# Kernel optimization log

Hardware: AMD Instinct MI355X
Metric: run time of the kernel (lower is better)

## Reference

```python
import jax, jax.numpy as jnp
import numpy as np

D_MODEL = 1024
NUM_HEADS = 16
HEAD_DIM = D_MODEL // NUM_HEADS


def setup_inputs() -> dict:
    key = jax.random.key(0)
    ks = jax.random.split(key, 6)
    B, S = 2, 2048
    w_scale = 1.0 / np.sqrt(D_MODEL)  # keep logits O(1) so the naive exp-softmax is stable
    return {
        "x": jax.random.normal(ks[0], (B, S, D_MODEL), dtype=jnp.float32),
        "y": jax.random.normal(ks[1], (B, S, D_MODEL), dtype=jnp.float32),
        "mask": jnp.zeros((S, S), dtype=jnp.float32),
        "Wq": jax.random.normal(ks[2], (D_MODEL, D_MODEL), dtype=jnp.float32) * w_scale,
        "Wk": jax.random.normal(ks[3], (D_MODEL, D_MODEL), dtype=jnp.float32) * w_scale,
        "Wv": jax.random.normal(ks[4], (D_MODEL, D_MODEL), dtype=jnp.float32) * w_scale,
        "Wo": jax.random.normal(ks[5], (D_MODEL, D_MODEL), dtype=jnp.float32) * w_scale,
    }


def _naive_softmax(s):
    # faithful to nirmalya_softmax: plain exp, sum + eps, no max subtraction
    p1 = jnp.exp(s)
    p2 = jnp.sum(p1, axis=-1, keepdims=True) + 1e-10
    return p1 / p2


def reference(x, y, mask, Wq, Wk, Wv, Wo):
    B, S, _ = x.shape
    # nn.Linear(bias=False): t @ W.T ; split heads -> [B, H, S, Dh]
    def split_heads(t):
        return t.reshape(B, S, NUM_HEADS, HEAD_DIM).transpose(0, 2, 1, 3)

    k = split_heads(x @ Wk.T)
    v = split_heads(x @ Wv.T)
    q = split_heads(y @ Wq.T)

    scores = jnp.einsum("bhqd,bhkd->bhqk", q, k) / np.sqrt(HEAD_DIM)
    scores = scores + mask  # [S,S] broadcasts over [B,H,S,S] (same math as permute-add-permute)
    attn = _naive_softmax(scores)
    out = jnp.einsum("bhqk,bhkd->bhqd", attn, v)  # [B,H,S,Dh]
    out = out.transpose(0, 2, 1, 3).reshape(B, S, D_MODEL)
    return out @ Wo.T
```

## Files before the change

### kernel.cpp

```cpp
#include <hip/hip_runtime.h>
#include <stdint.h>

typedef unsigned short u16;
typedef __attribute__((ext_vector_type(4))) float f32x4;
typedef __attribute__((ext_vector_type(8))) __bf16 bf16x8;
typedef __attribute__((ext_vector_type(4))) u16 u16x4;

#define AS1 __attribute__((address_space(1)))
#define AS3 __attribute__((address_space(3)))
#define GLOAD_LDS16(gp, lp) \
  __builtin_amdgcn_global_load_lds((const AS1 void*)(gp), (AS3 void*)(lp), 16, 0, 0)

__device__ __forceinline__ u16 f2bf(float f) {
  union { float f; unsigned u; } v; v.f = f;
  return (u16)((v.u + 0x7FFFu + ((v.u >> 16) & 1u)) >> 16);
}

__global__ __launch_bounds__(256) void convert_all(
    const float* __restrict__ x, const float* __restrict__ y,
    const float* __restrict__ wq, const float* __restrict__ wk,
    const float* __restrict__ wv, const float* __restrict__ wo,
    u16* __restrict__ xb, u16* __restrict__ yb, u16* __restrict__ wqb,
    u16* __restrict__ wkb, u16* __restrict__ wvb, u16* __restrict__ wob) {
  size_t i = (size_t)blockIdx.x * 256 + threadIdx.x;
  const float* src; u16* dst; float scale = 1.0f; size_t off;
  if (i < (size_t)(1u << 20)) { src = x; dst = xb; off = i; }
  else if (i < (size_t)(2u << 20)) { src = y; dst = yb; off = i - (1u << 20); }
  else {
    size_t j = i - (size_t)(2u << 20);
    unsigned w = (unsigned)(j >> 18); off = j & ((1u << 18) - 1);
    if (w == 0)      { src = wq; dst = wqb; scale = 0.125f; }
    else if (w == 1) { src = wk; dst = wkb; }
    else if (w == 2) { src = wv; dst = wvb; }
    else             { src = wo; dst = wob; }
  }
  f32x4 v = ((const f32x4*)src)[off];
  u16x4 r;
  r.x = f2bf(v.x * scale); r.y = f2bf(v.y * scale);
  r.z = f2bf(v.z * scale); r.w = f2bf(v.w * scale);
  ((u16x4*)dst)[off] = r;
}

template <int MODE>
__global__ __launch_bounds__(256, 2) void gemm_bt(
    const u16* __restrict__ A, const u16* __restrict__ Bt,
    void* __restrict__ C, int M, int N) {
  constexpr int K = 1024;
  __shared__ __align__(16) u16 As[128 * 32];
  __shared__ __align__(16) u16 Bs[128 * 32];
  const int tid = threadIdx.x;
  const int wave = tid >> 6, lane = tid & 63;
  const int l15 = lane & 15, quad = lane >> 4;
  const int tm = blockIdx.y * 128, tn = blockIdx.x * 128;
  const int wr = wave >> 1, wc = wave & 1;

  const int srow = wave * 32 + (lane >> 2);
  const int scol = (lane & 3) * 8;
  const u16* Ag = A + (size_t)(tm + srow) * K + scol;
  const u16* Bg = Bt + (size_t)(tn + srow) * K + scol;
  u16* Asl0 = &As[(wave * 2 + 0) * 512];
  u16* Asl1 = &As[(wave * 2 + 1) * 512];
  u16* Bsl0 = &Bs[(wave * 2 + 0) * 512];
  u16* Bsl1 = &Bs[(wave * 2 + 1) * 512];

  f32x4 acc[4][4] = {};

  for (int k0 = 0; k0 < K; k0 += 32) {
    __syncthreads();
    GLOAD_LDS16(Ag + k0, Asl0);
    GLOAD_LDS16(Ag + 16 * K + k0, Asl1);
    GLOAD_LDS16(Bg + k0, Bsl0);
    GLOAD_LDS16(Bg + 16 * K + k0, Bsl1);
    __syncthreads();
    bf16x8 af[4], bfr[4];
#pragma unroll
    for (int mi = 0; mi < 4; ++mi)
      af[mi] = *(const bf16x8*)&As[(wr * 64 + mi * 16 + l15) * 32 + quad * 8];
#pragma unroll
    for (int ni = 0; ni < 4; ++ni)
      bfr[ni] = *(const bf16x8*)&Bs[(wc * 64 + ni * 16 + l15) * 32 + quad * 8];
#pragma unroll
    for (int mi = 0; mi < 4; ++mi)
#pragma unroll
      for (int ni = 0; ni < 4; ++ni)
        acc[mi][ni] = __builtin_amdgcn_mfma_f32_16x16x32_bf16(
            af[mi], bfr[ni], acc[mi][ni], 0, 0, 0);
  }

#pragma unroll
  for (int mi = 0; mi < 4; ++mi) {
#pragma unroll
    for (int ni = 0; ni < 4; ++ni) {
#pragma unroll
      for (int r = 0; r < 4; ++r) {
        int gm = tm + wr * 64 + mi * 16 + quad * 4 + r;
        int gn = tn + wc * 64 + ni * 16 + l15;
        float val = acc[mi][ni][r];
        if (MODE == 0) {
          int b = gm >> 11, s = gm & 2047, h = gn >> 6, dh = gn & 63;
          ((u16*)C)[(((size_t)(b * 16 + h) * 2048 + s) << 6) + dh] = f2bf(val);
        } else if (MODE == 1) {
          int h = gm >> 6, dh = gm & 63, b = gn >> 11, s = gn & 2047;
          ((u16*)C)[(((size_t)(b * 16 + h) * 64 + dh) << 11) + s] = f2bf(val);
        } else {
          ((float*)C)[(size_t)gm * 1024 + gn] = val;
        }
      }
    }
  }
  (void)M; (void)N;
}

__global__ __launch_bounds__(256, 2) void attn_kernel(
    const u16* __restrict__ Qw, const u16* __restrict__ Kw,
    const u16* __restrict__ Vtw, const float* __restrict__ mask,
    u16* __restrict__ Ow) {
  constexpr int S = 2048;
  __shared__ __align__(16) u16 Ks[128 * 64];
  __shared__ __align__(16) u16 Vs[64 * 128];
  __shared__ __align__(16) u16 Ps[128 * 136];
  const int tid = threadIdx.x;
  const int wave = tid >> 6, lane = tid & 63;
  const int l15 = lane & 15, quad = lane >> 4;
  const int qt = blockIdx.x, h = blockIdx.y, b = blockIdx.z;
  const size_t head = ((size_t)(b * 16 + h)) * S * 64;

  bf16x8 aq[2][2];
#pragma unroll
  for (int mi = 0; mi < 2; ++mi)
#pragma unroll
    for (int kq = 0; kq < 2; ++kq)
      aq[mi][kq] = *(const bf16x8*)&Qw[head +
          (size_t)(qt * 128 + wave * 32 + mi * 16 + l15) * 64 + kq * 32 + quad * 8];

  __bf16 one_bf = (__bf16)1.0f;
  bf16x8 ones = {one_bf, one_bf, one_bf, one_bf, one_bf, one_bf, one_bf, one_bf};

  f32x4 oa[2][4] = {};
  f32x4 den[2] = {};

  const int krow = lane >> 3, kcol = (lane & 7) * 8;
  const int vrow = lane >> 4, vcol = (lane & 15) * 8;

  for (int kt = 0; kt < S; kt += 128) {
    __syncthreads();
#pragma unroll
    for (int c = 0; c < 4; ++c) {
      int g = wave * 4 + c;
      GLOAD_LDS16(&Kw[head + (size_t)(kt + g * 8 + krow) * 64 + kcol], &Ks[g * 512]);
    }
#pragma unroll
    for (int c = 0; c < 4; ++c) {
      int g = wave * 4 + c;
      GLOAD_LDS16(&Vtw[head + (size_t)(g * 4 + vrow) * S + kt + vcol], &Vs[g * 512]);
    }
    __syncthreads();

    f32x4 sa[2][8] = {};
#pragma unroll
    for (int kq = 0; kq < 2; ++kq) {
#pragma unroll
      for (int ni = 0; ni < 8; ++ni) {
        bf16x8 bk = *(const bf16x8*)&Ks[(ni * 16 + l15) * 64 + kq * 32 + quad * 8];
#pragma unroll
        for (int mi = 0; mi < 2; ++mi)
          sa[mi][ni] = __builtin_amdgcn_mfma_f32_16x16x32_bf16(
              aq[mi][kq], bk, sa[mi][ni], 0, 0, 0);
      }
    }

#pragma unroll
    for (int mi = 0; mi < 2; ++mi) {
#pragma unroll
      for (int ni = 0; ni < 8; ++ni) {
        int prow = wave * 32 + mi * 16 + quad * 4;
        int pcol = ni * 16 + l15;
        const float* mp = mask + (size_t)(qt * 128 + prow) * S + kt + pcol;
#pragma unroll
        for (int r = 0; r < 4; ++r) {
          float p = __expf(sa[mi][ni][r] + mp[(size_t)r * S]);
          Ps[(prow + r) * 136 + pcol] = f2bf(p);
        }
      }
    }

#pragma unroll
    for (int kq2 = 0; kq2 < 4; ++kq2) {
      bf16x8 ap[2];
#pragma unroll
      for (int mi = 0; mi < 2; ++mi)
        ap[mi] = *(const bf16x8*)&Ps[(wave * 32 + mi * 16 + l15) * 136 + kq2 * 32 + quad * 8];
#pragma unroll
      for (int ni = 0; ni < 4; ++ni) {
        bf16x8 bv = *(const bf16x8*)&Vs[(ni * 16 + l15) * 128 + kq2 * 32 + quad * 8];
#pragma unroll
        for (int mi = 0; mi < 2; ++mi)
          oa[mi][ni] = __builtin_amdgcn_mfma_f32_16x16x32_bf16(
              ap[mi], bv, oa[mi][ni], 0, 0, 0);
      }
#pragma unroll
      for (int mi = 0; mi < 2; ++mi)
        den[mi] = __builtin_amdgcn_mfma_f32_16x16x32_bf16(
            ap[mi], ones, den[mi], 0, 0, 0);
    }
  }

#pragma unroll
  for (int mi = 0; mi < 2; ++mi) {
#pragma unroll
    for (int ni = 0; ni < 4; ++ni) {
#pragma unroll
      for (int r = 0; r < 4; ++r) {
        int srow = qt * 128 + wave * 32 + mi * 16 + quad * 4 + r;
        int dh = ni * 16 + l15;
        float val = oa[mi][ni][r] / (den[mi][r] + 1e-10f);
        Ow[((size_t)(b * S + srow) << 10) + h * 64 + dh] = f2bf(val);
      }
    }
  }
}

extern "C" void kernel_launch(void* const* d_in, const int* in_sizes, int n_in,
                              void* d_out, int out_size, void* d_ws, size_t ws_size,
                              hipStream_t stream) {
  const float* x    = (const float*)d_in[0];
  const float* y    = (const float*)d_in[1];
  const float* mask = (const float*)d_in[2];
  const float* Wq   = (const float*)d_in[3];
  const float* Wk   = (const float*)d_in[4];
  const float* Wv   = (const float*)d_in[5];
  const float* Wo   = (const float*)d_in[6];
  char* ws = (char*)d_ws;
  const size_t MB = (size_t)1 << 20;
  u16* xb  = (u16*)(ws + 0  * MB);
  u16* yb  = (u16*)(ws + 8  * MB);
  u16* wqb = (u16*)(ws + 16 * MB);
  u16* wkb = (u16*)(ws + 18 * MB);
  u16* wvb = (u16*)(ws + 20 * MB);
  u16* wob = (u16*)(ws + 22 * MB);
  u16* Qw  = (u16*)(ws + 24 * MB);
  u16* Kw  = (u16*)(ws + 32 * MB);
  u16* Vtw = (u16*)(ws + 40 * MB);
  u16* Ow  = (u16*)(ws + 48 * MB);

  convert_all<<<12288, 256, 0, stream>>>(x, y, Wq, Wk, Wv, Wo,
                                         xb, yb, wqb, wkb, wvb, wob);
  gemm_bt<0><<<dim3(8, 32), 256, 0, stream>>>(yb, wqb, (void*)Qw, 4096, 1024);
  gemm_bt<0><<<dim3(8, 32), 256, 0, stream>>>(xb, wkb, (void*)Kw, 4096, 1024);
  gemm_bt<1><<<dim3(32, 8), 256, 0, stream>>>(wvb, xb, (void*)Vtw, 1024, 4096);
  attn_kernel<<<dim3(16, 16, 2), 256, 0, stream>>>(Qw, Kw, Vtw, mask, Ow);
  gemm_bt<2><<<dim3(8, 32), 256, 0, stream>>>(Ow, wob, d_out, 4096, 1024);
  (void)in_sizes; (void)n_in; (void)out_size; (void)ws_size;
}
```

Baseline: 288.8 us.

## Fuse QKV GEMMs, swizzle LDS, shrink attention tiles, vectorize mask and packing

Merges the three Q/K/V projection GEMMs into one launch with a z-dimension selector. Adds XOR swizzles to the GEMM and attention LDS layouts to avoid bank conflicts. Restructures attention to 64 query rows per block (16 per wave), computing S^T so that each lane holds four consecutive keys; this allows vectorized float4 mask loads issued before the barrier and packed bf16 stores into P. It also uses the hardware packed bf16 conversion when available and raises occupancy to 3 blocks per SM, at the cost of less K/V reuse per block and doubling the number of blocks.

```diff
diff --git a/kernel.cpp b/kernel.cpp
--- a/kernel.cpp
+++ b/kernel.cpp
@@ -3,6 +3,7 @@
 
 typedef unsigned short u16;
 typedef __attribute__((ext_vector_type(4))) float f32x4;
+typedef __attribute__((ext_vector_type(2))) __bf16 bf16x2;
 typedef __attribute__((ext_vector_type(8))) __bf16 bf16x8;
 typedef __attribute__((ext_vector_type(4))) u16 u16x4;
 
@@ -14,6 +15,17 @@
 __device__ __forceinline__ u16 f2bf(float f) {
   union { float f; unsigned u; } v; v.f = f;
   return (u16)((v.u + 0x7FFFu + ((v.u >> 16) & 1u)) >> 16);
+}
+
+__device__ __forceinline__ u16x4 pack4(float a, float b, float c, float d) {
+#if __has_builtin(__builtin_amdgcn_cvt_pk_bf16_f32)
+  union { struct { bf16x2 lo, hi; } p; u16x4 v; } u;
+  u.p.lo = __builtin_amdgcn_cvt_pk_bf16_f32(a, b);
+  u.p.hi = __builtin_amdgcn_cvt_pk_bf16_f32(c, d);
+  return u.v;
+#else
+  u16x4 r; r.x = f2bf(a); r.y = f2bf(b); r.z = f2bf(c); r.w = f2bf(d); return r;
+#endif
 }
 
 __global__ __launch_bounds__(256) void convert_all(
@@ -35,35 +47,24 @@
     else             { src = wo; dst = wob; }
   }
   f32x4 v = ((const f32x4*)src)[off];
-  u16x4 r;
-  r.x = f2bf(v.x * scale); r.y = f2bf(v.y * scale);
-  r.z = f2bf(v.z * scale); r.w = f2bf(v.w * scale);
-  ((u16x4*)dst)[off] = r;
-}
-
-template <int MODE>
-__global__ __launch_bounds__(256, 2) void gemm_bt(
-    const u16* __restrict__ A, const u16* __restrict__ Bt,
-    void* __restrict__ C, int M, int N) {
+  ((u16x4*)dst)[off] = pack4(v.x * scale, v.y * scale, v.z * scale, v.w * scale);
+}
+
+__device__ __forceinline__ void gemm_core(
+    const u16* __restrict__ A, const u16* __restrict__ Bt, int tm, int tn,
+    u16* As, u16* Bs, f32x4 acc[4][4], int wave, int lane) {
   constexpr int K = 1024;
-  __shared__ __align__(16) u16 As[128 * 32];
-  __shared__ __align__(16) u16 Bs[128 * 32];
-  const int tid = threadIdx.x;
-  const int wave = tid >> 6, lane = tid & 63;
-  const int l15 = lane & 15, quad = lane >> 4;
-  const int tm = blockIdx.y * 128, tn = blockIdx.x * 128;
+  const int l15 = lane & 15, quad = lane >> 4;
   const int wr = wave >> 1, wc = wave & 1;
-
-  const int srow = wave * 32 + (lane >> 2);
-  const int scol = (lane & 3) * 8;
-  const u16* Ag = A + (size_t)(tm + srow) * K + scol;
-  const u16* Bg = Bt + (size_t)(tn + srow) * K + scol;
+  const int srow = lane >> 2;
+  const int scol = ((lane & 3) ^ ((lane >> 3) & 3)) * 8;
+  const u16* Ag = A + (size_t)(tm + wave * 32 + srow) * K + scol;
+  const u16* Bg = Bt + (size_t)(tn + wave * 32 + srow) * K + scol;
   u16* Asl0 = &As[(wave * 2 + 0) * 512];
   u16* Asl1 = &As[(wave * 2 + 1) * 512];
   u16* Bsl0 = &Bs[(wave * 2 + 0) * 512];
   u16* Bsl1 = &Bs[(wave * 2 + 1) * 512];
-
-  f32x4 acc[4][4] = {};
+  const int rc = (quad ^ ((l15 >> 1) & 3)) * 8;
 
   for (int k0 = 0; k0 < K; k0 += 32) {
     __syncthreads();
@@ -75,10 +76,10 @@
     bf16x8 af[4], bfr[4];
 #pragma unroll
     for (int mi = 0; mi < 4; ++mi)
-      af[mi] = *(const bf16x8*)&As[(wr * 64 + mi * 16 + l15) * 32 + quad * 8];
+      af[mi] = *(const bf16x8*)&As[(wr * 64 + mi * 16 + l15) * 32 + rc];
 #pragma unroll
     for (int ni = 0; ni < 4; ++ni)
-      bfr[ni] = *(const bf16x8*)&Bs[(wc * 64 + ni * 16 + l15) * 32 + quad * 8];
+      bfr[ni] = *(const bf16x8*)&Bs[(wc * 64 + ni * 16 + l15) * 32 + rc];
 #pragma unroll
     for (int mi = 0; mi < 4; ++mi)
 #pragma unroll
@@ -86,6 +87,26 @@
         acc[mi][ni] = __builtin_amdgcn_mfma_f32_16x16x32_bf16(
             af[mi], bfr[ni], acc[mi][ni], 0, 0, 0);
   }
+}
+
+__global__ __launch_bounds__(256, 2) void qkv_gemm(
+    const u16* __restrict__ xb, const u16* __restrict__ yb,
+    const u16* __restrict__ wqb, const u16* __restrict__ wkb,
+    const u16* __restrict__ wvb,
+    u16* __restrict__ Qw, u16* __restrict__ Kw, u16* __restrict__ Vtw) {
+  __shared__ __align__(16) u16 As[128 * 32];
+  __shared__ __align__(16) u16 Bs[128 * 32];
+  const int tid = threadIdx.x, wave = tid >> 6, lane = tid & 63;
+  const int l15 = lane & 15, quad = lane >> 4;
+  const int wr = wave >> 1, wc = wave & 1;
+  const int z = blockIdx.z;
+  const u16 *A, *Bt; int tm, tn;
+  if (z == 0)      { A = yb;  Bt = wqb; tm = blockIdx.y * 128; tn = blockIdx.x * 128; }
+  else if (z == 1) { A = xb;  Bt = wkb; tm = blockIdx.y * 128; tn = blockIdx.x * 128; }
+  else             { A = wvb; Bt = xb;  tm = blockIdx.x * 128; tn = blockIdx.y * 128; }
+
+  f32x4 acc[4][4] = {};
+  gemm_core(A, Bt, tm, tn, As, Bs, acc, wave, lane);
 
 #pragma unroll
   for (int mi = 0; mi < 4; ++mi) {
@@ -95,127 +116,139 @@
       for (int r = 0; r < 4; ++r) {
         int gm = tm + wr * 64 + mi * 16 + quad * 4 + r;
         int gn = tn + wc * 64 + ni * 16 + l15;
-        float val = acc[mi][ni][r];
-        if (MODE == 0) {
+        u16 val = f2bf(acc[mi][ni][r]);
+        if (z == 2) {
+          int h = gm >> 6, dh = gm & 63, b = gn >> 11, s = gn & 2047;
+          Vtw[(((size_t)(b * 16 + h) * 64 + dh) << 11) + s] = val;
+        } else {
           int b = gm >> 11, s = gm & 2047, h = gn >> 6, dh = gn & 63;
-          ((u16*)C)[(((size_t)(b * 16 + h) * 2048 + s) << 6) + dh] = f2bf(val);
-        } else if (MODE == 1) {
-          int h = gm >> 6, dh = gm & 63, b = gn >> 11, s = gn & 2047;
-          ((u16*)C)[(((size_t)(b * 16 + h) * 64 + dh) << 11) + s] = f2bf(val);
-        } else {
-          ((float*)C)[(size_t)gm * 1024 + gn] = val;
+          u16* dst = (z == 0) ? Qw : Kw;
+          dst[(((size_t)(b * 16 + h) * 2048 + s) << 6) + dh] = val;
         }
       }
     }
   }
-  (void)M; (void)N;
-}
-
-__global__ __launch_bounds__(256, 2) void attn_kernel(
+}
+
+__global__ __launch_bounds__(256, 2) void out_gemm(
+    const u16* __restrict__ Ow, const u16* __restrict__ wob,
+    float* __restrict__ C) {
+  __shared__ __align__(16) u16 As[128 * 32];
+  __shared__ __align__(16) u16 Bs[128 * 32];
+  const int tid = threadIdx.x, wave = tid >> 6, lane = tid & 63;
+  const int l15 = lane & 15, quad = lane >> 4;
+  const int wr = wave >> 1, wc = wave & 1;
+  const int tm = blockIdx.y * 128, tn = blockIdx.x * 128;
+
+  f32x4 acc[4][4] = {};
+  gemm_core(Ow, wob, tm, tn, As, Bs, acc, wave, lane);
+
+#pragma unroll
+  for (int mi = 0; mi < 4; ++mi)
+#pragma unroll
+    for (int ni = 0; ni < 4; ++ni)
+#pragma unroll
+      for (int r = 0; r < 4; ++r) {
+        int gm = tm + wr * 64 + mi * 16 + quad * 4 + r;
+        int gn = tn + wc * 64 + ni * 16 + l15;
+        C[(size_t)gm * 1024 + gn] = acc[mi][ni][r];
+      }
+}
+
+__global__ __launch_bounds__(256, 3) void attn_kernel(
     const u16* __restrict__ Qw, const u16* __restrict__ Kw,
     const u16* __restrict__ Vtw, const float* __restrict__ mask,
     u16* __restrict__ Ow) {
   constexpr int S = 2048;
+  constexpr int PADK = 136;
   __shared__ __align__(16) u16 Ks[128 * 64];
   __shared__ __align__(16) u16 Vs[64 * 128];
-  __shared__ __align__(16) u16 Ps[128 * 136];
+  __shared__ __align__(16) u16 Ps[64 * PADK];
   const int tid = threadIdx.x;
   const int wave = tid >> 6, lane = tid & 63;
   const int l15 = lane & 15, quad = lane >> 4;
   const int qt = blockIdx.x, h = blockIdx.y, b = blockIdx.z;
   const size_t head = ((size_t)(b * 16 + h)) * S * 64;
-
-  bf16x8 aq[2][2];
-#pragma unroll
-  for (int mi = 0; mi < 2; ++mi)
-#pragma unroll
-    for (int kq = 0; kq < 2; ++kq)
-      aq[mi][kq] = *(const bf16x8*)&Qw[head +
-          (size_t)(qt * 128 + wave * 32 + mi * 16 + l15) * 64 + kq * 32 + quad * 8];
-
-  __bf16 one_bf = (__bf16)1.0f;
-  bf16x8 ones = {one_bf, one_bf, one_bf, one_bf, one_bf, one_bf, one_bf, one_bf};
-
-  f32x4 oa[2][4] = {};
-  f32x4 den[2] = {};
-
-  const int krow = lane >> 3, kcol = (lane & 7) * 8;
-  const int vrow = lane >> 4, vcol = (lane & 15) * 8;
+  const int q_global = qt * 64 + wave * 16 + l15;
+
+  bf16x8 qf[2];
+#pragma unroll
+  for (int kq = 0; kq < 2; ++kq)
+    qf[kq] = *(const bf16x8*)&Qw[head + (size_t)q_global * 64 + kq * 32 + quad * 8];
+
+  const __bf16 one_bf = (__bf16)1.0f;
+  const bf16x8 ones = {one_bf, one_bf, one_bf, one_bf, one_bf, one_bf, one_bf, one_bf};
+
+  f32x4 oa[4] = {};
+  f32x4 den = {};
+
+  const int k_r = lane >> 3;
+  const int k_c = ((lane & 7) ^ ((lane >> 3) & 7)) * 8;
+  const int v_r = lane >> 4;
+  const int v_cbase = lane & 15;
+  const float* mrow = mask + (size_t)q_global * S;
 
   for (int kt = 0; kt < S; kt += 128) {
     __syncthreads();
 #pragma unroll
     for (int c = 0; c < 4; ++c) {
       int g = wave * 4 + c;
-      GLOAD_LDS16(&Kw[head + (size_t)(kt + g * 8 + krow) * 64 + kcol], &Ks[g * 512]);
+      GLOAD_LDS16(&Kw[head + (size_t)(kt + g * 8 + k_r) * 64 + k_c], &Ks[g * 512]);
     }
 #pragma unroll
     for (int c = 0; c < 4; ++c) {
       int g = wave * 4 + c;
-      GLOAD_LDS16(&Vtw[head + (size_t)(g * 4 + vrow) * S + kt + vcol], &Vs[g * 512]);
-    }
-    __syncthreads();
-
-    f32x4 sa[2][8] = {};
+      int dh = g * 4 + v_r;
+      int scb = (v_cbase ^ (dh & 15)) * 8;
+      GLOAD_LDS16(&Vtw[head + (size_t)dh * S + kt + scb], &Vs[g * 512]);
+    }
+    f32x4 mv[8];
+#pragma unroll
+    for (int mk = 0; mk < 8; ++mk)
+      mv[mk] = *(const f32x4*)&mrow[kt + mk * 16 + quad * 4];
+    __syncthreads();
+
+    f32x4 sa[8] = {};
 #pragma unroll
     for (int kq = 0; kq < 2; ++kq) {
 #pragma unroll
-      for (int ni = 0; ni < 8; ++ni) {
-        bf16x8 bk = *(const bf16x8*)&Ks[(ni * 16 + l15) * 64 + kq * 32 + quad * 8];
-#pragma unroll
-        for (int mi = 0; mi < 2; ++mi)
-          sa[mi][ni] = __builtin_amdgcn_mfma_f32_16x16x32_bf16(
-              aq[mi][kq], bk, sa[mi][ni], 0, 0, 0);
-      }
-    }
-
-#pragma unroll
-    for (int mi = 0; mi < 2; ++mi) {
-#pragma unroll
-      for (int ni = 0; ni < 8; ++ni) {
-        int prow = wave * 32 + mi * 16 + quad * 4;
-        int pcol = ni * 16 + l15;
-        const float* mp = mask + (size_t)(qt * 128 + prow) * S + kt + pcol;
-#pragma unroll
-        for (int r = 0; r < 4; ++r) {
-          float p = __expf(sa[mi][ni][r] + mp[(size_t)r * S]);
-          Ps[(prow + r) * 136 + pcol] = f2bf(p);
-        }
-      }
+      for (int mk = 0; mk < 8; ++mk) {
+        int row = mk * 16 + l15;
+        bf16x8 ak = *(const bf16x8*)&Ks[row * 64 + (((kq * 4 + quad) ^ (l15 & 7)) * 8)];
+        sa[mk] = __builtin_amdgcn_mfma_f32_16x16x32_bf16(ak, qf[kq], sa[mk], 0, 0, 0);
+      }
+    }
+
+#pragma unroll
+    for (int mk = 0; mk < 8; ++mk) {
+      float p0 = __expf(sa[mk][0] + mv[mk][0]);
+      float p1 = __expf(sa[mk][1] + mv[mk][1]);
+      float p2 = __expf(sa[mk][2] + mv[mk][2]);
+      float p3 = __expf(sa[mk][3] + mv[mk][3]);
+      *(u16x4*)&Ps[(wave * 16 + l15) * PADK + mk * 16 + quad * 4] = pack4(p0, p1, p2, p3);
     }
 
 #pragma unroll
     for (int kq2 = 0; kq2 < 4; ++kq2) {
-      bf16x8 ap[2];
-#pragma unroll
-      for (int mi = 0; mi < 2; ++mi)
-        ap[mi] = *(const bf16x8*)&Ps[(wave * 32 + mi * 16 + l15) * 136 + kq2 * 32 + quad * 8];
-#pragma unroll
-      for (int ni = 0; ni < 4; ++ni) {
-        bf16x8 bv = *(const bf16x8*)&Vs[(ni * 16 + l15) * 128 + kq2 * 32 + quad * 8];
-#pragma unroll
-        for (int mi = 0; mi < 2; ++mi)
-          oa[mi][ni] = __builtin_amdgcn_mfma_f32_16x16x32_bf16(
-              ap[mi], bv, oa[mi][ni], 0, 0, 0);
-      }
-#pragma unroll
-      for (int mi = 0; mi < 2; ++mi)
-        den[mi] = __builtin_amdgcn_mfma_f32_16x16x32_bf16(
-            ap[mi], ones, den[mi], 0, 0, 0);
-    }
-  }
-
-#pragma unroll
-  for (int mi = 0; mi < 2; ++mi) {
-#pragma unroll
-    for (int ni = 0; ni < 4; ++ni) {
-#pragma unroll
-      for (int r = 0; r < 4; ++r) {
-        int srow = qt * 128 + wave * 32 + mi * 16 + quad * 4 + r;
-        int dh = ni * 16 + l15;
-        float val = oa[mi][ni][r] / (den[mi][r] + 1e-10f);
-        Ow[((size_t)(b * S + srow) << 10) + h * 64 + dh] = f2bf(val);
-      }
+      bf16x8 ap = *(const bf16x8*)&Ps[(wave * 16 + l15) * PADK + kq2 * 32 + quad * 8];
+#pragma unroll
+      for (int nv = 0; nv < 4; ++nv) {
+        int row = nv * 16 + l15;
+        bf16x8 bv = *(const bf16x8*)&Vs[row * 128 + (((kq2 * 4 + quad) ^ l15) * 8)];
+        oa[nv] = __builtin_amdgcn_mfma_f32_16x16x32_bf16(ap, bv, oa[nv], 0, 0, 0);
+      }
+      den = __builtin_amdgcn_mfma_f32_16x16x32_bf16(ap, ones, den, 0, 0, 0);
+    }
+  }
+
+#pragma unroll
+  for (int nv = 0; nv < 4; ++nv) {
+#pragma unroll
+    for (int r = 0; r < 4; ++r) {
+      int srow = qt * 64 + wave * 16 + quad * 4 + r;
+      int dh = nv * 16 + l15;
+      float val = oa[nv][r] / (den[r] + 1e-10f);
+      Ow[((size_t)(b * S + srow) << 10) + h * 64 + dh] = f2bf(val);
     }
   }
 }
@@ -245,10 +278,8 @@
 
   convert_all<<<12288, 256, 0, stream>>>(x, y, Wq, Wk, Wv, Wo,
                                          xb, yb, wqb, wkb, wvb, wob);
-  gemm_bt<0><<<dim3(8, 32), 256, 0, stream>>>(yb, wqb, (void*)Qw, 4096, 1024);
-  gemm_bt<0><<<dim3(8, 32), 256, 0, stream>>>(xb, wkb, (void*)Kw, 4096, 1024);
-  gemm_bt<1><<<dim3(32, 8), 256, 0, stream>>>(wvb, xb, (void*)Vtw, 1024, 4096);
-  attn_kernel<<<dim3(16, 16, 2), 256, 0, stream>>>(Qw, Kw, Vtw, mask, Ow);
-  gemm_bt<2><<<dim3(8, 32), 256, 0, stream>>>(Ow, wob, d_out, 4096, 1024);
+  qkv_gemm<<<dim3(8, 32, 3), 256, 0, stream>>>(xb, yb, wqb, wkb, wvb, Qw, Kw, Vtw);
+  attn_kernel<<<dim3(32, 16, 2), 256, 0, stream>>>(Qw, Kw, Vtw, mask, Ow);
+  out_gemm<<<dim3(8, 32), 256, 0, stream>>>(Ow, wob, (float*)d_out);
   (void)in_sizes; (void)n_in; (void)out_size; (void)ws_size;
 }
```

New measurement: 267.5 us. 7.4% less time.
